# Kernel tuning notes

Measured on AMD Instinct MI355X. Metric: run time of the kernel, lower is better.

Reference implementation:

```python
import jax, jax.numpy as jnp
import numpy as np

N, F_IN, HID, PERIODS, E = 50000, 8, 64, 12, 1200000


def _lin_init(k, fi, fo):
    # torch.nn.Linear default init: U(-1/sqrt(fi), 1/sqrt(fi))
    s = 1.0 / np.sqrt(fi)
    k1, k2 = jax.random.split(k)
    W = jax.random.uniform(k1, (fi, fo), minval=-s, maxval=s, dtype=jnp.float32)
    b = jax.random.uniform(k2, (fo,), minval=-s, maxval=s, dtype=jnp.float32)
    return W, b


def setup_inputs() -> dict:
    key = jax.random.key(0)
    ks = jax.random.split(key, 12)
    x = jax.random.normal(ks[0], (N, F_IN, PERIODS), dtype=jnp.float32)
    edge_index = jax.random.randint(ks[1], (2, E), 0, N, dtype=jnp.int64)
    edge_attr = jax.random.uniform(ks[2], (E,), dtype=jnp.float32)
    # GCNConv weights (glorot) + zero bias
    def gcn_init(k):
        s = np.sqrt(6.0 / (F_IN + HID))
        W = jax.random.uniform(k, (F_IN, HID), minval=-s, maxval=s, dtype=jnp.float32)
        return W, jnp.zeros((HID,), jnp.float32)
    Wcz, bcz = gcn_init(ks[3])
    Wcr, bcr = gcn_init(ks[4])
    Wch, bch = gcn_init(ks[5])
    # gate linears act on cat([conv_out, H]) -> 2*HID inputs
    Wlz, blz = _lin_init(ks[6], 2 * HID, HID)
    Wlr, blr = _lin_init(ks[7], 2 * HID, HID)
    Wlh, blh = _lin_init(ks[8], 2 * HID, HID)
    # temporal attention logits (uniform init as in A3TGCN)
    attention = jax.random.uniform(ks[9], (PERIODS,), dtype=jnp.float32)
    # outer readout Linear(HID, PERIODS)
    Wout, bout = _lin_init(ks[10], HID, PERIODS)
    return {"x": x, "edge_index": edge_index, "edge_attr": edge_attr,
            "attention": attention,
            "Wcz": Wcz, "bcz": bcz, "Wcr": Wcr, "bcr": bcr, "Wch": Wch, "bch": bch,
            "Wlz": Wlz, "blz": blz, "Wlr": Wlr, "blr": blr, "Wlh": Wlh, "blh": blh,
            "Wout": Wout, "bout": bout}


def reference(x, edge_index, edge_attr, attention,
              Wcz, bcz, Wcr, bcr, Wch, bch,
              Wlz, blz, Wlr, blr, Wlh, blh,
              Wout, bout):
    n = x.shape[0]
    src, dst = edge_index[0], edge_index[1]
    # GCN symmetric normalization with self-loops (self-loop weight = 1)
    deg = jax.ops.segment_sum(edge_attr, dst, num_segments=n) + 1.0
    dinv = jax.lax.rsqrt(deg)                      # [N]
    norm = dinv[src] * edge_attr * dinv[dst]       # [E]
    self_norm = (dinv * dinv)[:, None]             # [N,1]

    def gcn(xt, W, b):
        xw = xt @ W                                # [N,HID]
        agg = jax.ops.segment_sum(xw[src] * norm[:, None], dst, num_segments=n)
        return agg + xw * self_norm + b

    H0 = jnp.zeros((n, Wcz.shape[1]), x.dtype)     # A3TGCN passes H=None each period
    probs = jax.nn.softmax(attention)

    def period_step(acc, inp):
        xt, p = inp                                # xt: [N,F_IN]
        Z = jax.nn.sigmoid(jnp.concatenate([gcn(xt, Wcz, bcz), H0], axis=1) @ Wlz + blz)
        R = jax.nn.sigmoid(jnp.concatenate([gcn(xt, Wcr, bcr), H0], axis=1) @ Wlr + blr)
        Ht = jnp.tanh(jnp.concatenate([gcn(xt, Wch, bch), H0 * R], axis=1) @ Wlh + blh)
        H = Z * H0 + (1.0 - Z) * Ht
        return acc + p * H, None

    xs = jnp.moveaxis(x, 2, 0)                     # [PERIODS, N, F_IN]
    H_accum, _ = jax.lax.scan(period_step, jnp.zeros_like(H0), (xs, probs))
    h = jax.nn.relu(H_accum)
    return h @ Wout + bout                         # [N, PERIODS]
```

## Files before the change

kernel.cpp:

```cpp
#include <hip/hip_runtime.h>
#include <hip/hip_fp16.h>
#include <cmath>

#define F_IN 8
#define PER 12
#define FEAT 96
#define HID 64
#define CAP 64
#define NB 8
#define BINBITS 8
#define BINCAP 7168
#define EPB 2048

static inline size_t al256(size_t x) { return (x + 255) & ~(size_t)255; }

__device__ __forceinline__ float frcp(float x) { return __builtin_amdgcn_rcpf(x); }


__global__ void k_weights(const float* __restrict__ Wcz, const float* __restrict__ bcz,
                          const float* __restrict__ Wch, const float* __restrict__ bch,
                          const float* __restrict__ Wlz, const float* __restrict__ blz,
                          const float* __restrict__ Wlh, const float* __restrict__ blh,
                          const float* __restrict__ att, float* __restrict__ M,
                          int* __restrict__ cursor) {
    int j = threadIdx.x;
    cursor[j] = 0;
    if (j < HID) {
        for (int f = 0; f < F_IN; ++f) {
            float az = 0.f, ah = 0.f;
            for (int k = 0; k < HID; ++k) {
                az = fmaf(Wcz[f * HID + k], Wlz[k * HID + j], az);
                ah = fmaf(Wch[f * HID + k], Wlh[k * HID + j], ah);
            }
            M[f * HID + j] = az;
            M[512 + f * HID + j] = ah;
        }
        float cz = blz[j], ch = blh[j];
        for (int k = 0; k < HID; ++k) {
            cz = fmaf(bcz[k], Wlz[k * HID + j], cz);
            ch = fmaf(bch[k], Wlh[k * HID + j], ch);
        }
        M[1024 + j] = cz;
        M[1088 + j] = ch;
        if (j < PER) {
            float s = 0.f;
            for (int t = 0; t < PER; ++t) s += expf(att[t]);
            M[1152 + j] = expf(att[j]) / s;
        }
    }
}


__global__ __launch_bounds__(256) void k_pass1(const int* __restrict__ src, const int* __restrict__ dst,
                                               const float* __restrict__ attr,
                                               int* __restrict__ cursor, int2* __restrict__ binned, int e) {
    __shared__ int hist[256];
    __shared__ int base[256];
    int t = threadIdx.x;
    int blockstart = blockIdx.x * EPB;
    hist[t] = 0;
    __syncthreads();
    int2 ent[8];
    int  br[8];
#pragma unroll
    for (int r = 0; r < 8; ++r) {
        int i = blockstart + r * 256 + t;
        if (i < e) {
            int d = dst[i];
            int b = d >> BINBITS;
            int rank = atomicAdd(&hist[b], 1);
            ent[r].x = src[i] | ((d & 255) << 20);
            ent[r].y = __float_as_int(attr[i]);
            br[r] = (b << 13) | rank;
        } else br[r] = -1;
    }
    __syncthreads();
    int h = hist[t];
    if (h > 0) base[t] = atomicAdd(&cursor[t], h);
    __syncthreads();
#pragma unroll
    for (int r = 0; r < 8; ++r) {
        if (br[r] >= 0) {
            int b = br[r] >> 13, rank = br[r] & 8191;
            int pos = base[b] + rank;
            if (pos < BINCAP)
                binned[(size_t)b * BINCAP + pos] = ent[r];
        }
    }
}


__global__ __launch_bounds__(256) void k_pass2(const int* __restrict__ cursor, const int2* __restrict__ binned,
                                               int2* __restrict__ bucket, int* __restrict__ cnt,
                                               float* __restrict__ dinv_g, int n) {
    __shared__ int   hist[256];
    __shared__ float wsum[256];
    int b = blockIdx.x;
    int t = threadIdx.x;
    hist[t] = 0;
    wsum[t] = 0.f;
    __syncthreads();
    int m = min(cursor[b], BINCAP);
    const int2* bin = binned + (size_t)b * BINCAP;
    for (int i = t; i < m; i += 256) {
        int2 p = bin[i];
        int dl = (p.x >> 20) & 255;
        atomicAdd(&wsum[dl], __int_as_float(p.y));
        int rank = atomicAdd(&hist[dl], 1);
        if (rank < CAP) {
            int d = (b << BINBITS) | dl;
            bucket[(size_t)d * CAP + rank] = make_int2(p.x & 0xFFFFF, p.y);
        }
    }
    __syncthreads();
    int node = (b << BINBITS) | t;
    if (node < n) {
        cnt[node] = hist[t];
        dinv_g[node] = rsqrtf(1.0f + wsum[t]);
    }
}


__global__ void k_xhalf(const float4* __restrict__ X4, const float* __restrict__ dinv,
                        uint2* __restrict__ Xh2, int total4) {
    int i = blockIdx.x * 256 + threadIdx.x;
    if (i >= total4) return;
    int node = i / 24;
    float s = dinv[node];
    float4 v = X4[i];
    __half2 a = __floats2half2_rn(s * v.x, s * v.y);
    __half2 b = __floats2half2_rn(s * v.z, s * v.w);
    uint2 o;
    o.x = __builtin_bit_cast(unsigned int, a);
    o.y = __builtin_bit_cast(unsigned int, b);
    Xh2[i] = o;
}


__global__ void k_zero(int* __restrict__ cnt, int n) {
    int i = blockIdx.x * 256 + threadIdx.x;
    if (i < n) cnt[i] = 0;
}

__global__ void k_bucket(const int* __restrict__ src, const int* __restrict__ dst,
                         const float* __restrict__ attr,
                         int* __restrict__ cnt, int2* __restrict__ bucket, int e) {
    int i = blockIdx.x * 256 + threadIdx.x;
    if (i >= e) return;
    int d = dst[i];
    int pos = atomicAdd(&cnt[d], 1);
    if (pos < CAP) {
        int2 p;
        p.x = src[i];
        p.y = __float_as_int(attr[i]);
        bucket[(size_t)d * CAP + pos] = p;
    }
}

__global__ void k_dinv(const int* __restrict__ cnt, const int2* __restrict__ bucket,
                       float* __restrict__ dinv, int n) {
    int gid = blockIdx.x * 256 + threadIdx.x;
    int node = gid >> 6;
    int lane = gid & 63;
    if (node >= n) return;
    int c = min(cnt[node], CAP);
    float s = (lane < c) ? __int_as_float(bucket[(size_t)node * CAP + lane].y) : 0.f;
#pragma unroll
    for (int d = 32; d; d >>= 1) s += __shfl_xor(s, d);
    if (lane == 0) dinv[node] = rsqrtf(1.0f + s);
}


#define EDGE_FMA(ew, rr)                                                     \
    {                                                                        \
        float w_ = __int_as_float((ew).y);                                   \
        float2 a_ = __half22float2(__builtin_bit_cast(__half2, (rr).x));     \
        float2 b_ = __half22float2(__builtin_bit_cast(__half2, (rr).y));     \
        accA.x = fmaf(w_, a_.x, accA.x);                                     \
        accA.y = fmaf(w_, a_.y, accA.y);                                     \
        accA.z = fmaf(w_, b_.x, accA.z);                                     \
        accA.w = fmaf(w_, b_.y, accA.w);                                     \
    }
#define EDGE_FMA_B(ew, rr)                                                   \
    {                                                                        \
        float w_ = __int_as_float((ew).y);                                   \
        float2 a_ = __half22float2(__builtin_bit_cast(__half2, (rr).x));     \
        float2 b_ = __half22float2(__builtin_bit_cast(__half2, (rr).y));     \
        accB.x = fmaf(w_, a_.x, accB.x);                                     \
        accB.y = fmaf(w_, a_.y, accB.y);                                     \
        accB.z = fmaf(w_, b_.x, accB.z);                                     \
        accB.w = fmaf(w_, b_.y, accB.w);                                     \
    }

__global__ __launch_bounds__(256) void k_fused(const int* __restrict__ cnt,
                                               const int2* __restrict__ bucket,
                                               const float* __restrict__ dinv,
                                               const uint2* __restrict__ Xh2,
                                               const float* __restrict__ M,
                                               const float* __restrict__ Wout,
                                               const float* __restrict__ bout,
                                               float* __restrict__ out, int n) {
    __shared__ int2  s_ew[NB][CAP];
    __shared__ int   s_cnt[NB];
    __shared__ float s_dv[NB];
    __shared__ float s_xp[NB][104];
    __shared__ float s_acc[NB][HID + 1];
    int t = threadIdx.x;
    int node0 = blockIdx.x * NB;

    if (t < NB) {
        int node = node0 + t;
        s_cnt[t] = (node < n) ? min(cnt[node], CAP) : 0;
        s_dv[t]  = (node < n) ? dinv[node] : 0.f;
    }
    __syncthreads();

#pragma unroll
    for (int idx = t; idx < NB * CAP; idx += 256) {
        int ln = idx >> 6;
        int e  = idx & (CAP - 1);
        if (e < s_cnt[ln]) {
            int2 p = bucket[(size_t)(node0 + ln) * CAP + e];
            s_ew[ln][e] = make_int2(p.x * 24, p.y);
        }
    }
    __syncthreads();

    {
        int g32 = t >> 5;
        int l = t & 31;
        int node = node0 + g32;
        if (node < n && l < 24) {
            float dv = s_dv[g32];
            int c = s_cnt[g32];
            uint2 sh = Xh2[(size_t)node * 24 + l];
            float4 accA = make_float4(0.f, 0.f, 0.f, 0.f);
            float4 accB = make_float4(0.f, 0.f, 0.f, 0.f);
            int e = 0;
            if (c >= 4) {
                int2  ce0 = s_ew[g32][0], ce1 = s_ew[g32][1], ce2 = s_ew[g32][2], ce3 = s_ew[g32][3];
                uint2 cr0 = Xh2[(size_t)ce0.x + l];
                uint2 cr1 = Xh2[(size_t)ce1.x + l];
                uint2 cr2 = Xh2[(size_t)ce2.x + l];
                uint2 cr3 = Xh2[(size_t)ce3.x + l];
                for (; e + 8 <= c; e += 4) {
                    int2  ne0 = s_ew[g32][e + 4], ne1 = s_ew[g32][e + 5];
                    int2  ne2 = s_ew[g32][e + 6], ne3 = s_ew[g32][e + 7];
                    uint2 nr0 = Xh2[(size_t)ne0.x + l];
                    uint2 nr1 = Xh2[(size_t)ne1.x + l];
                    uint2 nr2 = Xh2[(size_t)ne2.x + l];
                    uint2 nr3 = Xh2[(size_t)ne3.x + l];
                    EDGE_FMA(ce0, cr0); EDGE_FMA_B(ce1, cr1);
                    EDGE_FMA(ce2, cr2); EDGE_FMA_B(ce3, cr3);
                    ce0 = ne0; ce1 = ne1; ce2 = ne2; ce3 = ne3;
                    cr0 = nr0; cr1 = nr1; cr2 = nr2; cr3 = nr3;
                }
                EDGE_FMA(ce0, cr0); EDGE_FMA_B(ce1, cr1);
                EDGE_FMA(ce2, cr2); EDGE_FMA_B(ce3, cr3);
                e += 4;
            }
            for (; e < c; ++e) {
                int2 e0 = s_ew[g32][e];
                uint2 r0 = Xh2[(size_t)e0.x + l];
                EDGE_FMA(e0, r0);
            }
            float2 sa = __half22float2(__builtin_bit_cast(__half2, sh.x));
            float2 sb = __half22float2(__builtin_bit_cast(__half2, sh.y));
            float4 r;
            r.x = dv * (sa.x + accA.x + accB.x);
            r.y = dv * (sa.y + accA.y + accB.y);
            r.z = dv * (sb.x + accA.z + accB.z);
            r.w = dv * (sb.y + accA.w + accB.w);
            *(float4*)&s_xp[g32][l * 4] = r;
        }
    }
    __syncthreads();

    {
        int lane = t & 63;
        int wv = t >> 6;
        float mz[F_IN], mh[F_IN];
#pragma unroll
        for (int f = 0; f < F_IN; ++f) {
            mz[f] = M[f * HID + lane];
            mh[f] = M[512 + f * HID + lane];
        }
        float cz = M[1024 + lane], ch = M[1088 + lane];
        float pr[PER];
#pragma unroll
        for (int tt = 0; tt < PER; ++tt) pr[tt] = M[1152 + tt];

#pragma unroll
        for (int q = 0; q < 2; ++q) {
            int ln = wv * 2 + q;
            if (node0 + ln < n) {
                float acc = 0.f;
#pragma unroll
                for (int tt = 0; tt < PER; ++tt) {
                    float xz = cz, xh = ch;
#pragma unroll
                    for (int f = 0; f < F_IN; ++f) {
                        float xv = s_xp[ln][f * PER + tt];
                        xz = fmaf(xv, mz[f], xz);
                        xh = fmaf(xv, mh[f], xh);
                    }
                    float z  = frcp(1.f + __expf(-xz));
                    float th = 1.f - 2.f * frcp(__expf(2.f * xh) + 1.f);
                    acc += pr[tt] * (1.f - z) * th;
                }
                s_acc[ln][lane] = fmaxf(acc, 0.f);
            }
        }
    }
    __syncthreads();

    if (t < NB * PER) {
        int ln = t / PER;
        int pp = t - ln * PER;
        int node = node0 + ln;
        if (node < n) {
            float o = bout[pp];
#pragma unroll
            for (int j = 0; j < HID; ++j) o = fmaf(s_acc[ln][j], Wout[j * PER + pp], o);
            out[(size_t)node * PER + pp] = o;
        }
    }
}


extern "C" void kernel_launch(void* const* d_in, const int* in_sizes, int n_in,
                              void* d_out, int out_size, void* d_ws, size_t ws_size,
                              hipStream_t stream) {
    const float* X     = (const float*)d_in[0];
    const int*   ei    = (const int*)d_in[1];
    const float* attr  = (const float*)d_in[2];
    const float* att   = (const float*)d_in[3];
    const float* Wcz   = (const float*)d_in[4];
    const float* bcz   = (const float*)d_in[5];
    const float* Wch   = (const float*)d_in[8];
    const float* bch   = (const float*)d_in[9];
    const float* Wlz   = (const float*)d_in[10];
    const float* blz   = (const float*)d_in[11];
    const float* Wlh   = (const float*)d_in[14];
    const float* blh   = (const float*)d_in[15];
    const float* Wout  = (const float*)d_in[16];
    const float* bout  = (const float*)d_in[17];
    float* out = (float*)d_out;

    const int N = in_sizes[0] / FEAT;
    const int E = in_sizes[2];
    const int* src = ei;
    const int* dst = ei + E;

    const int NBINS = (N + 255) >> 8;
    const int total4 = N * (FEAT / 4);

    char* base = (char*)d_ws;
    size_t o = 0;
    int*   cnt    = (int*)  (base + o); o += al256((size_t)N * 4);
    float* dinv   = (float*)(base + o); o += al256((size_t)N * 4);
    float* M      = (float*)(base + o); o += al256(1280 * 4);
    int2*  bucket = (int2*) (base + o); o += al256((size_t)N * CAP * 8);
    uint2* Xh2    = (uint2*)(base + o); o += al256((size_t)N * FEAT * 2);
    int*   cursor = (int*)  (base + o); o += al256(256 * 4);
    int2*  binned = (int2*) (base + o);
    size_t need_sorted = o + al256((size_t)NBINS * BINCAP * 8);

    if (ws_size >= need_sorted && N <= 50176 && NBINS <= 256) {
        k_weights<<<1, 256, 0, stream>>>(Wcz, bcz, Wch, bch, Wlz, blz, Wlh, blh, att, M, cursor);
        k_pass1<<<(E + EPB - 1) / EPB, 256, 0, stream>>>(src, dst, attr, cursor, binned, E);
        k_pass2<<<NBINS, 256, 0, stream>>>(cursor, binned, bucket, cnt, dinv, N);
        k_xhalf<<<(total4 + 255) / 256, 256, 0, stream>>>((const float4*)X, dinv, Xh2, total4);
    } else {
        k_weights<<<1, 256, 0, stream>>>(Wcz, bcz, Wch, bch, Wlz, blz, Wlh, blh, att, M, cursor);
        k_zero<<<(N + 255) / 256, 256, 0, stream>>>(cnt, N);
        k_bucket<<<(E + 255) / 256, 256, 0, stream>>>(src, dst, attr, cnt, bucket, E);
        k_dinv<<<((N * 64) + 255) / 256, 256, 0, stream>>>(cnt, bucket, dinv, N);
        k_xhalf<<<(total4 + 255) / 256, 256, 0, stream>>>((const float4*)X, dinv, Xh2, total4);
    }

    int blocks = (N + NB - 1) / NB;
    k_fused<<<blocks, 256, 0, stream>>>(cnt, bucket, dinv, Xh2, M, Wout, bout, out, N);
}
```

Baseline: 124.8 us.

## Fuse half-precision X conversion into pass2, use fma_mix, parallelize weight precompute

```diff
diff --git a/kernel.cpp b/kernel.cpp
--- a/kernel.cpp
+++ b/kernel.cpp
@@ -9,12 +9,18 @@
 #define CAP 64
 #define NB 8
 #define BINBITS 8
+#define NPB 256
 #define BINCAP 7168
 #define EPB 2048
 
 static inline size_t al256(size_t x) { return (x + 255) & ~(size_t)255; }
 
 __device__ __forceinline__ float frcp(float x) { return __builtin_amdgcn_rcpf(x); }
+
+#define MIX_LO(acc, w, bits) \
+    asm("v_fma_mix_f32 %0, %1, %2, %0 op_sel_hi:[0,1,0]" : "+v"(acc) : "v"(w), "v"(bits))
+#define MIX_HI(acc, w, bits) \
+    asm("v_fma_mix_f32 %0, %1, %2, %0 op_sel:[0,1,0] op_sel_hi:[0,1,0]" : "+v"(acc) : "v"(w), "v"(bits))
 
 
 __global__ void k_weights(const float* __restrict__ Wcz, const float* __restrict__ bcz,
@@ -23,18 +29,22 @@
                           const float* __restrict__ Wlh, const float* __restrict__ blh,
                           const float* __restrict__ att, float* __restrict__ M,
                           int* __restrict__ cursor) {
-    int j = threadIdx.x;
-    cursor[j] = 0;
-    if (j < HID) {
-        for (int f = 0; f < F_IN; ++f) {
-            float az = 0.f, ah = 0.f;
-            for (int k = 0; k < HID; ++k) {
-                az = fmaf(Wcz[f * HID + k], Wlz[k * HID + j], az);
-                ah = fmaf(Wch[f * HID + k], Wlh[k * HID + j], ah);
-            }
-            M[f * HID + j] = az;
-            M[512 + f * HID + j] = ah;
-        }
+    int t = threadIdx.x;
+    int j = t & 63;
+    int w = t >> 6;
+    cursor[t] = 0;
+#pragma unroll
+    for (int q = 0; q < 2; ++q) {
+        int f = 2 * w + q;
+        float az = 0.f, ah = 0.f;
+        for (int k = 0; k < HID; ++k) {
+            az = fmaf(Wcz[f * HID + k], Wlz[k * HID + j], az);
+            ah = fmaf(Wch[f * HID + k], Wlh[k * HID + j], ah);
+        }
+        M[f * HID + j] = az;
+        M[512 + f * HID + j] = ah;
+    }
+    if (w == 0) {
         float cz = blz[j], ch = blh[j];
         for (int k = 0; k < HID; ++k) {
             cz = fmaf(bcz[k], Wlz[k * HID + j], cz);
@@ -44,7 +54,7 @@
         M[1088 + j] = ch;
         if (j < PER) {
             float s = 0.f;
-            for (int t = 0; t < PER; ++t) s += expf(att[t]);
+            for (int tt = 0; tt < PER; ++tt) s += expf(att[tt]);
             M[1152 + j] = expf(att[j]) / s;
         }
     }
@@ -90,11 +100,13 @@
 }
 
 
-__global__ __launch_bounds__(256) void k_pass2(const int* __restrict__ cursor, const int2* __restrict__ binned,
-                                               int2* __restrict__ bucket, int* __restrict__ cnt,
-                                               float* __restrict__ dinv_g, int n) {
-    __shared__ int   hist[256];
-    __shared__ float wsum[256];
+__global__ __launch_bounds__(256) void k_pass2x(const int* __restrict__ cursor, const int2* __restrict__ binned,
+                                                const float4* __restrict__ X4,
+                                                int2* __restrict__ bucket, int* __restrict__ cnt,
+                                                float* __restrict__ dinv_g, uint2* __restrict__ Xh2, int n) {
+    __shared__ int   hist[NPB];
+    __shared__ float wsum[NPB];
+    __shared__ float sdv[NPB];
     int b = blockIdx.x;
     int t = threadIdx.x;
     hist[t] = 0;
@@ -113,13 +125,67 @@
         }
     }
     __syncthreads();
-    int node = (b << BINBITS) | t;
-    if (node < n) {
-        cnt[node] = hist[t];
-        dinv_g[node] = rsqrtf(1.0f + wsum[t]);
-    }
-}
-
+    int node0 = b << BINBITS;
+    {
+        int node = node0 + t;
+        float dv = 0.f;
+        if (node < n) {
+            cnt[node] = hist[t];
+            dv = rsqrtf(1.0f + wsum[t]);
+            dinv_g[node] = dv;
+        }
+        sdv[t] = dv;
+    }
+    __syncthreads();
+    int nn = n - node0; if (nn > NPB) nn = NPB; if (nn < 0) nn = 0;
+    int lim = nn * 24;
+    size_t base4 = (size_t)node0 * 24;
+    for (int i = t; i < lim; i += 256) {
+        int nl = i / 24;
+        float s = sdv[nl];
+        float4 v = X4[base4 + i];
+        __half2 a = __floats2half2_rn(s * v.x, s * v.y);
+        __half2 c = __floats2half2_rn(s * v.z, s * v.w);
+        uint2 o;
+        o.x = __builtin_bit_cast(unsigned int, a);
+        o.y = __builtin_bit_cast(unsigned int, c);
+        Xh2[base4 + i] = o;
+    }
+}
+
+
+__global__ void k_zero(int* __restrict__ cnt, int n) {
+    int i = blockIdx.x * 256 + threadIdx.x;
+    if (i < n) cnt[i] = 0;
+}
+
+__global__ void k_bucket(const int* __restrict__ src, const int* __restrict__ dst,
+                         const float* __restrict__ attr,
+                         int* __restrict__ cnt, int2* __restrict__ bucket, int e) {
+    int i = blockIdx.x * 256 + threadIdx.x;
+    if (i >= e) return;
+    int d = dst[i];
+    int pos = atomicAdd(&cnt[d], 1);
+    if (pos < CAP) {
+        int2 p;
+        p.x = src[i];
+        p.y = __float_as_int(attr[i]);
+        bucket[(size_t)d * CAP + pos] = p;
+    }
+}
+
+__global__ void k_dinv(const int* __restrict__ cnt, const int2* __restrict__ bucket,
+                       float* __restrict__ dinv, int n) {
+    int gid = blockIdx.x * 256 + threadIdx.x;
+    int node = gid >> 6;
+    int lane = gid & 63;
+    if (node >= n) return;
+    int c = min(cnt[node], CAP);
+    float s = (lane < c) ? __int_as_float(bucket[(size_t)node * CAP + lane].y) : 0.f;
+#pragma unroll
+    for (int d = 32; d; d >>= 1) s += __shfl_xor(s, d);
+    if (lane == 0) dinv[node] = rsqrtf(1.0f + s);
+}
 
 __global__ void k_xhalf(const float4* __restrict__ X4, const float* __restrict__ dinv,
                         uint2* __restrict__ Xh2, int total4) {
@@ -137,59 +203,21 @@
 }
 
 
-__global__ void k_zero(int* __restrict__ cnt, int n) {
-    int i = blockIdx.x * 256 + threadIdx.x;
-    if (i < n) cnt[i] = 0;
-}
-
-__global__ void k_bucket(const int* __restrict__ src, const int* __restrict__ dst,
-                         const float* __restrict__ attr,
-                         int* __restrict__ cnt, int2* __restrict__ bucket, int e) {
-    int i = blockIdx.x * 256 + threadIdx.x;
-    if (i >= e) return;
-    int d = dst[i];
-    int pos = atomicAdd(&cnt[d], 1);
-    if (pos < CAP) {
-        int2 p;
-        p.x = src[i];
-        p.y = __float_as_int(attr[i]);
-        bucket[(size_t)d * CAP + pos] = p;
-    }
-}
-
-__global__ void k_dinv(const int* __restrict__ cnt, const int2* __restrict__ bucket,
-                       float* __restrict__ dinv, int n) {
-    int gid = blockIdx.x * 256 + threadIdx.x;
-    int node = gid >> 6;
-    int lane = gid & 63;
-    if (node >= n) return;
-    int c = min(cnt[node], CAP);
-    float s = (lane < c) ? __int_as_float(bucket[(size_t)node * CAP + lane].y) : 0.f;
-#pragma unroll
-    for (int d = 32; d; d >>= 1) s += __shfl_xor(s, d);
-    if (lane == 0) dinv[node] = rsqrtf(1.0f + s);
-}
-
-
-#define EDGE_FMA(ew, rr)                                                     \
-    {                                                                        \
-        float w_ = __int_as_float((ew).y);                                   \
-        float2 a_ = __half22float2(__builtin_bit_cast(__half2, (rr).x));     \
-        float2 b_ = __half22float2(__builtin_bit_cast(__half2, (rr).y));     \
-        accA.x = fmaf(w_, a_.x, accA.x);                                     \
-        accA.y = fmaf(w_, a_.y, accA.y);                                     \
-        accA.z = fmaf(w_, b_.x, accA.z);                                     \
-        accA.w = fmaf(w_, b_.y, accA.w);                                     \
-    }
-#define EDGE_FMA_B(ew, rr)                                                   \
-    {                                                                        \
-        float w_ = __int_as_float((ew).y);                                   \
-        float2 a_ = __half22float2(__builtin_bit_cast(__half2, (rr).x));     \
-        float2 b_ = __half22float2(__builtin_bit_cast(__half2, (rr).y));     \
-        accB.x = fmaf(w_, a_.x, accB.x);                                     \
-        accB.y = fmaf(w_, a_.y, accB.y);                                     \
-        accB.z = fmaf(w_, b_.x, accB.z);                                     \
-        accB.w = fmaf(w_, b_.y, accB.w);                                     \
+#define EDGEA(ew, rr)                                  \
+    {                                                  \
+        float w_ = __int_as_float((ew).y);             \
+        MIX_LO(accA0, w_, (rr).x);                     \
+        MIX_HI(accA1, w_, (rr).x);                     \
+        MIX_LO(accA2, w_, (rr).y);                     \
+        MIX_HI(accA3, w_, (rr).y);                     \
+    }
+#define EDGEB(ew, rr)                                  \
+    {                                                  \
+        float w_ = __int_as_float((ew).y);             \
+        MIX_LO(accB0, w_, (rr).x);                     \
+        MIX_HI(accB1, w_, (rr).x);                     \
+        MIX_LO(accB2, w_, (rr).y);                     \
+        MIX_HI(accB3, w_, (rr).y);                     \
     }
 
 __global__ __launch_bounds__(256) void k_fused(const int* __restrict__ cnt,
@@ -234,8 +262,8 @@
             float dv = s_dv[g32];
             int c = s_cnt[g32];
             uint2 sh = Xh2[(size_t)node * 24 + l];
-            float4 accA = make_float4(0.f, 0.f, 0.f, 0.f);
-            float4 accB = make_float4(0.f, 0.f, 0.f, 0.f);
+            float accA0 = 0.f, accA1 = 0.f, accA2 = 0.f, accA3 = 0.f;
+            float accB0 = 0.f, accB1 = 0.f, accB2 = 0.f, accB3 = 0.f;
             int e = 0;
             if (c >= 4) {
                 int2  ce0 = s_ew[g32][0], ce1 = s_ew[g32][1], ce2 = s_ew[g32][2], ce3 = s_ew[g32][3];
@@ -250,27 +278,27 @@
                     uint2 nr1 = Xh2[(size_t)ne1.x + l];
                     uint2 nr2 = Xh2[(size_t)ne2.x + l];
                     uint2 nr3 = Xh2[(size_t)ne3.x + l];
-                    EDGE_FMA(ce0, cr0); EDGE_FMA_B(ce1, cr1);
-                    EDGE_FMA(ce2, cr2); EDGE_FMA_B(ce3, cr3);
+                    EDGEA(ce0, cr0); EDGEB(ce1, cr1);
+                    EDGEA(ce2, cr2); EDGEB(ce3, cr3);
                     ce0 = ne0; ce1 = ne1; ce2 = ne2; ce3 = ne3;
                     cr0 = nr0; cr1 = nr1; cr2 = nr2; cr3 = nr3;
                 }
-                EDGE_FMA(ce0, cr0); EDGE_FMA_B(ce1, cr1);
-                EDGE_FMA(ce2, cr2); EDGE_FMA_B(ce3, cr3);
+                EDGEA(ce0, cr0); EDGEB(ce1, cr1);
+                EDGEA(ce2, cr2); EDGEB(ce3, cr3);
                 e += 4;
             }
             for (; e < c; ++e) {
                 int2 e0 = s_ew[g32][e];
                 uint2 r0 = Xh2[(size_t)e0.x + l];
-                EDGE_FMA(e0, r0);
+                EDGEA(e0, r0);
             }
             float2 sa = __half22float2(__builtin_bit_cast(__half2, sh.x));
             float2 sb = __half22float2(__builtin_bit_cast(__half2, sh.y));
             float4 r;
-            r.x = dv * (sa.x + accA.x + accB.x);
-            r.y = dv * (sa.y + accA.y + accB.y);
-            r.z = dv * (sb.x + accA.z + accB.z);
-            r.w = dv * (sb.y + accA.w + accB.w);
+            r.x = dv * (sa.x + accA0 + accB0);
+            r.y = dv * (sa.y + accA1 + accB1);
+            r.z = dv * (sb.x + accA2 + accB2);
+            r.w = dv * (sb.y + accA3 + accB3);
             *(float4*)&s_xp[g32][l * 4] = r;
         }
     }
@@ -304,9 +332,9 @@
                         xz = fmaf(xv, mz[f], xz);
                         xh = fmaf(xv, mh[f], xh);
                     }
-                    float z  = frcp(1.f + __expf(-xz));
-                    float th = 1.f - 2.f * frcp(__expf(2.f * xh) + 1.f);
-                    acc += pr[tt] * (1.f - z) * th;
+                    float zb = frcp(1.f + __expf(xz));
+                    float th = fmaf(-2.f, frcp(__expf(2.f * xh) + 1.f), 1.f);
+                    acc = fmaf(pr[tt], zb * th, acc);
                 }
                 s_acc[ln][lane] = fmaxf(acc, 0.f);
             }
@@ -352,7 +380,7 @@
     const int* src = ei;
     const int* dst = ei + E;
 
-    const int NBINS = (N + 255) >> 8;
+    const int NBINS  = (N + NPB - 1) >> BINBITS;
     const int total4 = N * (FEAT / 4);
 
     char* base = (char*)d_ws;
@@ -366,11 +394,10 @@
     int2*  binned = (int2*) (base + o);
     size_t need_sorted = o + al256((size_t)NBINS * BINCAP * 8);
 
-    if (ws_size >= need_sorted && N <= 50176 && NBINS <= 256) {
+    if (ws_size >= need_sorted && NBINS <= 256 && N < (1 << 20)) {
         k_weights<<<1, 256, 0, stream>>>(Wcz, bcz, Wch, bch, Wlz, blz, Wlh, blh, att, M, cursor);
         k_pass1<<<(E + EPB - 1) / EPB, 256, 0, stream>>>(src, dst, attr, cursor, binned, E);
-        k_pass2<<<NBINS, 256, 0, stream>>>(cursor, binned, bucket, cnt, dinv, N);
-        k_xhalf<<<(total4 + 255) / 256, 256, 0, stream>>>((const float4*)X, dinv, Xh2, total4);
+        k_pass2x<<<NBINS, 256, 0, stream>>>(cursor, binned, (const float4*)X, bucket, cnt, dinv, Xh2, N);
     } else {
         k_weights<<<1, 256, 0, stream>>>(Wcz, bcz, Wch, bch, Wlz, blz, Wlh, blh, att, M, cursor);
         k_zero<<<(N + 255) / 256, 256, 0, stream>>>(cnt, N);
```

Result: faster. 113.7 us (-8.9%).
